# Kernel optimization log

Hardware: AMD Instinct MI355X
Metric: run time of the kernel (lower is better)

Reference implementation:

```python
import jax, jax.numpy as jnp
import numpy as np

GAMMA = 0.99      # discount_factor
LAM = 0.95        # gae_decay
CLIP = 0.2        # clipping_param
LOG_2PI = float(np.log(2.0 * np.pi))

B, T, A = 512, 2048, 16


def setup_inputs() -> dict:
    key = jax.random.key(0)
    ks = jax.random.split(key, 8)
    rewards = jax.random.normal(ks[0], (B, T), dtype=jnp.float32)
    critic_out = jax.random.normal(ks[1], (B, T + 1), dtype=jnp.float32)
    mu = jax.random.normal(ks[2], (B, T, A), dtype=jnp.float32)
    sigma = jax.random.uniform(ks[3], (B, T, A), dtype=jnp.float32) * 0.5 + 0.5
    old_mu = jax.random.normal(ks[4], (B, T, A), dtype=jnp.float32)
    old_sigma = jax.random.uniform(ks[5], (B, T, A), dtype=jnp.float32) * 0.5 + 0.5
    actions = jax.random.normal(ks[6], (B, T, A), dtype=jnp.float32)
    dones = jax.random.randint(ks[7], (B, T), 0, 2, dtype=jnp.int32)
    return {"rewards": rewards, "critic_out": critic_out, "mu": mu, "sigma": sigma,
            "old_mu": old_mu, "old_sigma": old_sigma, "actions": actions, "dones": dones}


def _normal_log_prob(x, mu, sigma):
    return -jnp.log(sigma) - 0.5 * LOG_2PI - 0.5 * jnp.square((x - mu) / sigma)


def _gae(rewards, dones_f, critic_out):
    # td_residuals: rewards + gamma * V[1:] - V[:-1]   -> [B, T]
    td = rewards + GAMMA * critic_out[:, 1:] - critic_out[:, :-1]
    b, t = rewards.shape
    # Reversed recurrence: adv[t] = td[t] + gamma*lam*(1 - done[t+1]) * adv[t+1],
    # for t = T-2 .. 0; adv[T-1] stays 0 (matches original loop bounds).
    xs = (jnp.flip(td[:, : t - 1], axis=1).T,        # [T-1, B]
          jnp.flip(dones_f[:, 1:], axis=1).T)        # [T-1, B]

    def step(carry, x):
        td_t, d_t = x
        adv = td_t + GAMMA * LAM * (1.0 - d_t) * carry
        return adv, adv

    _, advs = jax.lax.scan(step, jnp.zeros((b,), rewards.dtype), xs)
    advs = jnp.flip(advs, axis=0).T                  # [B, T-1]
    return jnp.concatenate([advs, jnp.zeros((b, 1), rewards.dtype)], axis=1)


def reference(rewards, critic_out, mu, sigma, old_mu, old_sigma, actions, dones):
    dones_f = dones.astype(rewards.dtype)
    advantages = _gae(rewards, dones_f, critic_out)          # [B, T]
    lp = _normal_log_prob(actions, mu, sigma)                # [B, T, A]
    old_lp = _normal_log_prob(actions, old_mu, old_sigma)    # [B, T, A]
    ratio = jnp.exp(lp - old_lp)
    clipped = jnp.minimum(jnp.maximum(ratio, 1.0 + CLIP), 1.0 - CLIP)
    adv = advantages[..., None]                              # broadcast over action dim
    obj = jnp.minimum(adv * ratio, adv * clipped)
    entropy = jnp.log(sigma) + 0.5 + 0.5 * LOG_2PI           # Normal entropy, [B, T, A]
    return jnp.mean(obj) + entropy
```

## Files before the change

kernel.cpp:

```cpp
#include <hip/hip_runtime.h>
#include <math.h>

#define BB 512
#define TT 2048
#define AA 16
#define NTOT (512LL * 2048LL * 16LL)
#define GAMMA 0.99f
#define GLAM  0.9405f
#define ENTC  1.4189385332046727f

#define NB3 2048

typedef float f32x4 __attribute__((ext_vector_type(4)));

__device__ __forceinline__ float obj1(float x, float m, float s,
                                      float om, float os, float ad)
{
    float rs  = __builtin_amdgcn_rcpf(s);
    float ros = __builtin_amdgcn_rcpf(os);
    float z   = (x - m) * rs;
    float zo  = (x - om) * ros;
    float d   = 0.5f * (zo * zo - z * z);
    float ratio = os * rs * __expf(d);
    return fminf(ad * ratio, ad * 0.8f);
}

__device__ __forceinline__ double obj4d(f32x4 m, f32x4 s, f32x4 om, f32x4 os,
                                        f32x4 x, float ad)
{
    float o0 = obj1(x.x, m.x, s.x, om.x, os.x, ad);
    float o1 = obj1(x.y, m.y, s.y, om.y, os.y, ad);
    float o2 = obj1(x.z, m.z, s.z, om.z, os.z, ad);
    float o3 = obj1(x.w, m.w, s.w, om.w, os.w, ad);
    return (double)o0 + (double)o1 + (double)o2 + (double)o3;
}

__global__ __launch_bounds__(512, 4) void gae_obj_kernel(
    const float* __restrict__ rewards, const float* __restrict__ vout,
    const int* __restrict__ dones,
    const float* __restrict__ mu, const float* __restrict__ sigma,
    const float* __restrict__ old_mu, const float* __restrict__ old_sigma,
    const float* __restrict__ actions,
    double* __restrict__ partials)
{
    __shared__ float  adv_s[TT];
    __shared__ float  wA[8], wB[8];
    __shared__ double wsum[8];

    const int b    = blockIdx.x;
    const int tid  = threadIdx.x;
    const int lane = tid & 63;
    const int wave = tid >> 6;

    {
        const float* rw = rewards + (size_t)b * TT;
        const float* V  = vout    + (size_t)b * (TT + 1);
        const int*   dn = dones   + (size_t)b * TT;

        const int t_lo = TT - 4 - 4 * tid;

        f32x4 r4 = *(const f32x4*)(rw + t_lo);
        int4  d4 = *(const int4*)(dn + t_lo);
        int   dt = (tid == 0) ? 1 : dn[t_lo + 4];
        float vv[5];
        #pragma unroll
        for (int j = 0; j < 5; ++j) vv[j] = V[t_lo + j];

        float rr[4] = {r4.x, r4.y, r4.z, r4.w};
        int   dd[5] = {d4.x, d4.y, d4.z, d4.w, dt};

        float ak[4], bk[4];
        float SA = 1.f, SB = 0.f;
        #pragma unroll
        for (int k = 0; k < 4; ++k) {
            const int j = 3 - k;
            float bu = rr[j] + GAMMA * vv[j + 1] - vv[j];
            float au = GLAM * (1.f - (float)dd[j + 1]);
            if (k == 0 && tid == 0) { au = 0.f; bu = 0.f; }
            ak[k] = au; bk[k] = bu;
            SB = au * SB + bu;
            SA = au * SA;
        }

        #pragma unroll
        for (int off = 1; off < 64; off <<= 1) {
            float pA = __shfl_up(SA, off, 64);
            float pB = __shfl_up(SB, off, 64);
            if (lane >= off) { SB = SA * pB + SB; SA = SA * pA; }
        }

        if (lane == 63) { wA[wave] = SA; wB[wave] = SB; }
        __syncthreads();

        float PA = 1.f, PB = 0.f;
        for (int w = 0; w < wave; ++w) {
            float aw = wA[w], bw = wB[w];
            PB = aw * PB + bw;
            PA = aw * PA;
        }

        float EA = __shfl_up(SA, 1, 64);
        float EB = __shfl_up(SB, 1, 64);
        if (lane == 0) { EA = 1.f; EB = 0.f; }

        float x = EA * PB + EB;
        float outb[4];
        #pragma unroll
        for (int k = 0; k < 4; ++k) {
            x = ak[k] * x + bk[k];
            outb[3 - k] = x;
        }
        *(f32x4*)(adv_s + t_lo) = (f32x4){outb[0], outb[1], outb[2], outb[3]};
    }
    __syncthreads();

    const size_t rowf4 = (size_t)b * (TT * AA / 4);
    const f32x4* m4  = (const f32x4*)mu        + rowf4;
    const f32x4* s4  = (const f32x4*)sigma     + rowf4;
    const f32x4* om4 = (const f32x4*)old_mu    + rowf4;
    const f32x4* os4 = (const f32x4*)old_sigma + rowf4;
    const f32x4* x4  = (const f32x4*)actions   + rowf4;

    uint32_t f = (uint32_t)tid;
    f32x4 m0  = __builtin_nontemporal_load(m4 + f);
    f32x4 s0  = s4[f];
    f32x4 om0 = __builtin_nontemporal_load(om4 + f);
    f32x4 os0 = __builtin_nontemporal_load(os4 + f);
    f32x4 x0  = __builtin_nontemporal_load(x4 + f);
    float a0  = adv_s[f >> 2];

    double lsum = 0.0;
    #pragma unroll 1
    for (int it = 0; it < 15; ++it) {
        const uint32_t fn = f + 512u;
        f32x4 m1  = __builtin_nontemporal_load(m4 + fn);
        f32x4 s1  = s4[fn];
        f32x4 om1 = __builtin_nontemporal_load(om4 + fn);
        f32x4 os1 = __builtin_nontemporal_load(os4 + fn);
        f32x4 x1  = __builtin_nontemporal_load(x4 + fn);
        float a1  = adv_s[fn >> 2];

        lsum += obj4d(m0, s0, om0, os0, x0, a0);

        m0 = m1; s0 = s1; om0 = om1; os0 = os1; x0 = x1; a0 = a1; f = fn;
    }
    lsum += obj4d(m0, s0, om0, os0, x0, a0);

    #pragma unroll
    for (int off = 32; off > 0; off >>= 1)
        lsum += __shfl_down(lsum, off, 64);
    if (lane == 0) wsum[wave] = lsum;
    __syncthreads();
    if (tid == 0) {
        double t = 0.0;
        #pragma unroll
        for (int w = 0; w < 8; ++w) t += wsum[w];
        partials[b] = t;
    }
}

__global__ __launch_bounds__(256) void out_kernel(
    const float* __restrict__ sigma, const double* __restrict__ partials,
    float* __restrict__ out)
{
    const int tid  = threadIdx.x;
    const int lane = tid & 63, wave = tid >> 6;

    double s = partials[tid] + partials[tid + 256];
    #pragma unroll
    for (int off = 32; off > 0; off >>= 1)
        s += __shfl_down(s, off, 64);
    __shared__ double wsum[4];
    __shared__ float  mean_s;
    if (lane == 0) wsum[wave] = s;
    __syncthreads();
    if (tid == 0)
        mean_s = (float)((wsum[0] + wsum[1] + wsum[2] + wsum[3]) / (double)NTOT);
    __syncthreads();
    const float mean = mean_s;

    const uint32_t HALF = (uint32_t)(NTOT / 4 / 2);
    const uint32_t STEP = (uint32_t)NB3 * 256u;
    uint32_t v = (uint32_t)blockIdx.x * 256u + (uint32_t)tid;

    const f32x4* s4 = (const f32x4*)sigma;
    f32x4* o4 = (f32x4*)out;

    f32x4 a0 = s4[v];
    f32x4 b0 = s4[v + HALF];
    #pragma unroll 1
    for (int it = 0; it < 3; ++it) {
        const uint32_t vn = v + STEP;
        f32x4 a1 = s4[vn];
        f32x4 b1 = s4[vn + HALF];

        f32x4 oa, ob;
        oa.x = mean + __logf(a0.x) + ENTC;  oa.y = mean + __logf(a0.y) + ENTC;
        oa.z = mean + __logf(a0.z) + ENTC;  oa.w = mean + __logf(a0.w) + ENTC;
        ob.x = mean + __logf(b0.x) + ENTC;  ob.y = mean + __logf(b0.y) + ENTC;
        ob.z = mean + __logf(b0.z) + ENTC;  ob.w = mean + __logf(b0.w) + ENTC;
        __builtin_nontemporal_store(oa, o4 + v);
        __builtin_nontemporal_store(ob, o4 + v + HALF);

        a0 = a1; b0 = b1; v = vn;
    }
    f32x4 oa, ob;
    oa.x = mean + __logf(a0.x) + ENTC;  oa.y = mean + __logf(a0.y) + ENTC;
    oa.z = mean + __logf(a0.z) + ENTC;  oa.w = mean + __logf(a0.w) + ENTC;
    ob.x = mean + __logf(b0.x) + ENTC;  ob.y = mean + __logf(b0.y) + ENTC;
    ob.z = mean + __logf(b0.z) + ENTC;  ob.w = mean + __logf(b0.w) + ENTC;
    __builtin_nontemporal_store(oa, o4 + v);
    __builtin_nontemporal_store(ob, o4 + v + HALF);
}

extern "C" void kernel_launch(void* const* d_in, const int* in_sizes, int n_in,
                              void* d_out, int out_size, void* d_ws, size_t ws_size,
                              hipStream_t stream) {
    const float* rewards   = (const float*)d_in[0];
    const float* critic    = (const float*)d_in[1];
    const float* mu        = (const float*)d_in[2];
    const float* sigma     = (const float*)d_in[3];
    const float* old_mu    = (const float*)d_in[4];
    const float* old_sigma = (const float*)d_in[5];
    const float* actions   = (const float*)d_in[6];
    const int*   dones     = (const int*)d_in[7];
    float* out = (float*)d_out;

    double* partials = (double*)d_ws;

    gae_obj_kernel<<<BB, 512, 0, stream>>>(rewards, critic, dones,
                                           mu, sigma, old_mu, old_sigma,
                                           actions, partials);
    out_kernel<<<NB3, 256, 0, stream>>>(sigma, partials, out);
}
```

Measured before the change: 324.7 us.

## Split each batch row across four blocks and unroll fully-loaded output kernel

The objective kernel now launches four blocks per batch row. Each block recomputes the full GAE scan for its row, then processes one quarter of the row's elements with a two-stage manual software pipeline separated by sched_barriers. The goal is more blocks in flight to saturate HBM bandwidth, at the cost of running the scan redundantly four times per row. The output kernel doubles its grid, issues four independent loads per thread before any compute, and folds the entropy constant into the mean. It also reduces 2048 partials instead of 512.

```diff
diff --git a/kernel.cpp b/kernel.cpp
--- a/kernel.cpp
+++ b/kernel.cpp
@@ -9,7 +9,9 @@
 #define GLAM  0.9405f
 #define ENTC  1.4189385332046727f
 
-#define NB3 2048
+#define QPB 4
+#define NB1 (BB * QPB)
+#define NB3 4096
 
 typedef float f32x4 __attribute__((ext_vector_type(4)));
 
@@ -35,7 +37,7 @@
     return (double)o0 + (double)o1 + (double)o2 + (double)o3;
 }
 
-__global__ __launch_bounds__(512, 4) void gae_obj_kernel(
+__global__ __launch_bounds__(512) void gae_obj_kernel(
     const float* __restrict__ rewards, const float* __restrict__ vout,
     const int* __restrict__ dones,
     const float* __restrict__ mu, const float* __restrict__ sigma,
@@ -47,7 +49,8 @@
     __shared__ float  wA[8], wB[8];
     __shared__ double wsum[8];
 
-    const int b    = blockIdx.x;
+    const int b    = blockIdx.x >> 2;
+    const int q    = blockIdx.x & 3;
     const int tid  = threadIdx.x;
     const int lane = tid & 63;
     const int wave = tid >> 6;
@@ -114,37 +117,43 @@
     }
     __syncthreads();
 
-    const size_t rowf4 = (size_t)b * (TT * AA / 4);
-    const f32x4* m4  = (const f32x4*)mu        + rowf4;
-    const f32x4* s4  = (const f32x4*)sigma     + rowf4;
-    const f32x4* om4 = (const f32x4*)old_mu    + rowf4;
-    const f32x4* os4 = (const f32x4*)old_sigma + rowf4;
-    const f32x4* x4  = (const f32x4*)actions   + rowf4;
-
-    uint32_t f = (uint32_t)tid;
-    f32x4 m0  = __builtin_nontemporal_load(m4 + f);
-    f32x4 s0  = s4[f];
-    f32x4 om0 = __builtin_nontemporal_load(om4 + f);
-    f32x4 os0 = __builtin_nontemporal_load(os4 + f);
-    f32x4 x0  = __builtin_nontemporal_load(x4 + f);
-    float a0  = adv_s[f >> 2];
-
-    double lsum = 0.0;
-    #pragma unroll 1
-    for (int it = 0; it < 15; ++it) {
-        const uint32_t fn = f + 512u;
-        f32x4 m1  = __builtin_nontemporal_load(m4 + fn);
-        f32x4 s1  = s4[fn];
-        f32x4 om1 = __builtin_nontemporal_load(om4 + fn);
-        f32x4 os1 = __builtin_nontemporal_load(os4 + fn);
-        f32x4 x1  = __builtin_nontemporal_load(x4 + fn);
-        float a1  = adv_s[fn >> 2];
-
-        lsum += obj4d(m0, s0, om0, os0, x0, a0);
-
-        m0 = m1; s0 = s1; om0 = om1; os0 = os1; x0 = x1; a0 = a1; f = fn;
-    }
-    lsum += obj4d(m0, s0, om0, os0, x0, a0);
+    const size_t basef4 = (size_t)b * 8192 + (size_t)q * 2048;
+    const f32x4* m4  = (const f32x4*)mu        + basef4;
+    const f32x4* s4  = (const f32x4*)sigma     + basef4;
+    const f32x4* om4 = (const f32x4*)old_mu    + basef4;
+    const f32x4* os4 = (const f32x4*)old_sigma + basef4;
+    const f32x4* x4  = (const f32x4*)actions   + basef4;
+    const float* advq = adv_s + q * 512;
+
+    const uint32_t f0 = (uint32_t)tid;
+    const uint32_t f1 = f0 + 512u;
+    const uint32_t f2 = f0 + 1024u;
+    const uint32_t f3 = f0 + 1536u;
+
+    f32x4 Am, As, Aom, Aos, Ax; float Aa;
+    f32x4 Bm, Bs, Bom, Bos, Bx; float Ba;
+
+    auto LOADC = [&](uint32_t f, f32x4& m, f32x4& s, f32x4& om, f32x4& os,
+                     f32x4& x, float& a) {
+        m  = __builtin_nontemporal_load(m4 + f);
+        s  = s4[f];
+        om = __builtin_nontemporal_load(om4 + f);
+        os = __builtin_nontemporal_load(os4 + f);
+        x  = __builtin_nontemporal_load(x4 + f);
+        a  = advq[f >> 2];
+    };
+
+    LOADC(f0, Am, As, Aom, Aos, Ax, Aa);
+    LOADC(f1, Bm, Bs, Bom, Bos, Bx, Ba);
+    __builtin_amdgcn_sched_barrier(0);
+    double lsum = obj4d(Am, As, Aom, Aos, Ax, Aa);
+    LOADC(f2, Am, As, Aom, Aos, Ax, Aa);
+    __builtin_amdgcn_sched_barrier(0);
+    lsum += obj4d(Bm, Bs, Bom, Bos, Bx, Ba);
+    LOADC(f3, Bm, Bs, Bom, Bos, Bx, Ba);
+    __builtin_amdgcn_sched_barrier(0);
+    lsum += obj4d(Am, As, Aom, Aos, Ax, Aa);
+    lsum += obj4d(Bm, Bs, Bom, Bos, Bx, Ba);
 
     #pragma unroll
     for (int off = 32; off > 0; off >>= 1)
@@ -155,7 +164,7 @@
         double t = 0.0;
         #pragma unroll
         for (int w = 0; w < 8; ++w) t += wsum[w];
-        partials[b] = t;
+        partials[blockIdx.x] = t;
     }
 }
 
@@ -166,51 +175,48 @@
     const int tid  = threadIdx.x;
     const int lane = tid & 63, wave = tid >> 6;
 
-    double s = partials[tid] + partials[tid + 256];
+    double s = 0.0;
+    #pragma unroll
+    for (int i = 0; i < 8; ++i) s += partials[tid + 256 * i];
     #pragma unroll
     for (int off = 32; off > 0; off >>= 1)
         s += __shfl_down(s, off, 64);
     __shared__ double wsum[4];
-    __shared__ float  mean_s;
+    __shared__ float  mc_s;
     if (lane == 0) wsum[wave] = s;
     __syncthreads();
     if (tid == 0)
-        mean_s = (float)((wsum[0] + wsum[1] + wsum[2] + wsum[3]) / (double)NTOT);
-    __syncthreads();
-    const float mean = mean_s;
-
-    const uint32_t HALF = (uint32_t)(NTOT / 4 / 2);
-    const uint32_t STEP = (uint32_t)NB3 * 256u;
-    uint32_t v = (uint32_t)blockIdx.x * 256u + (uint32_t)tid;
+        mc_s = (float)((wsum[0] + wsum[1] + wsum[2] + wsum[3]) / (double)NTOT)
+               + ENTC;
+    __syncthreads();
+    const float mc = mc_s;
+
+    const uint32_t Q = (uint32_t)(NTOT / 4 / 4);
+    const uint32_t v = (uint32_t)blockIdx.x * 256u + (uint32_t)tid;
 
     const f32x4* s4 = (const f32x4*)sigma;
     f32x4* o4 = (f32x4*)out;
 
-    f32x4 a0 = s4[v];
-    f32x4 b0 = s4[v + HALF];
-    #pragma unroll 1
-    for (int it = 0; it < 3; ++it) {
-        const uint32_t vn = v + STEP;
-        f32x4 a1 = s4[vn];
-        f32x4 b1 = s4[vn + HALF];
-
-        f32x4 oa, ob;
-        oa.x = mean + __logf(a0.x) + ENTC;  oa.y = mean + __logf(a0.y) + ENTC;
-        oa.z = mean + __logf(a0.z) + ENTC;  oa.w = mean + __logf(a0.w) + ENTC;
-        ob.x = mean + __logf(b0.x) + ENTC;  ob.y = mean + __logf(b0.y) + ENTC;
-        ob.z = mean + __logf(b0.z) + ENTC;  ob.w = mean + __logf(b0.w) + ENTC;
-        __builtin_nontemporal_store(oa, o4 + v);
-        __builtin_nontemporal_store(ob, o4 + v + HALF);
-
-        a0 = a1; b0 = b1; v = vn;
-    }
-    f32x4 oa, ob;
-    oa.x = mean + __logf(a0.x) + ENTC;  oa.y = mean + __logf(a0.y) + ENTC;
-    oa.z = mean + __logf(a0.z) + ENTC;  oa.w = mean + __logf(a0.w) + ENTC;
-    ob.x = mean + __logf(b0.x) + ENTC;  ob.y = mean + __logf(b0.y) + ENTC;
-    ob.z = mean + __logf(b0.z) + ENTC;  ob.w = mean + __logf(b0.w) + ENTC;
+    f32x4 a = s4[v];
+    f32x4 b = s4[v + Q];
+    f32x4 c = s4[v + 2 * Q];
+    f32x4 d = s4[v + 3 * Q];
+    __builtin_amdgcn_sched_barrier(0);
+
+    f32x4 oa, ob, oc, od;
+    oa.x = mc + __logf(a.x);  oa.y = mc + __logf(a.y);
+    oa.z = mc + __logf(a.z);  oa.w = mc + __logf(a.w);
+    ob.x = mc + __logf(b.x);  ob.y = mc + __logf(b.y);
+    ob.z = mc + __logf(b.z);  ob.w = mc + __logf(b.w);
+    oc.x = mc + __logf(c.x);  oc.y = mc + __logf(c.y);
+    oc.z = mc + __logf(c.z);  oc.w = mc + __logf(c.w);
+    od.x = mc + __logf(d.x);  od.y = mc + __logf(d.y);
+    od.z = mc + __logf(d.z);  od.w = mc + __logf(d.w);
+
     __builtin_nontemporal_store(oa, o4 + v);
-    __builtin_nontemporal_store(ob, o4 + v + HALF);
+    __builtin_nontemporal_store(ob, o4 + v + Q);
+    __builtin_nontemporal_store(oc, o4 + v + 2 * Q);
+    __builtin_nontemporal_store(od, o4 + v + 3 * Q);
 }
 
 extern "C" void kernel_launch(void* const* d_in, const int* in_sizes, int n_in,
@@ -228,8 +234,8 @@
 
     double* partials = (double*)d_ws;
 
-    gae_obj_kernel<<<BB, 512, 0, stream>>>(rewards, critic, dones,
-                                           mu, sigma, old_mu, old_sigma,
-                                           actions, partials);
+    gae_obj_kernel<<<NB1, 512, 0, stream>>>(rewards, critic, dones,
+                                            mu, sigma, old_mu, old_sigma,
+                                            actions, partials);
     out_kernel<<<NB3, 256, 0, stream>>>(sigma, partials, out);
 }
```

Result: no change. 322.0 us (-0.8%).
